# Kernel optimization log

Measured on AMD Instinct MI355X. Metric: run time of the kernel, lower is better.

## Reference

```python
import jax, jax.numpy as jnp
import numpy as np

N = 100000   # nodes
E = 1600000  # edges (avg degree 16)
D = 128      # in_dim


def setup_inputs() -> dict:
    key = jax.random.key(0)
    k = jax.random.split(key, 8)
    h = jax.random.normal(k[0], (N, D), dtype=jnp.float32)
    d = jax.random.uniform(k[1], (N,), dtype=jnp.float32)  # per-node degree norm (e.g. deg^-0.5)
    yes_no = jax.random.uniform(k[2], (E,), dtype=jnp.float32)
    gate_w = jax.random.normal(k[3], (1, 2 * D), dtype=jnp.float32) * (1.414 / np.sqrt(2 * D))
    gate_b = jnp.zeros((1,), dtype=jnp.float32)
    yes_weight = jax.random.uniform(k[4], (), dtype=jnp.float32)
    no_weight = jax.random.uniform(k[5], (), dtype=jnp.float32)
    src = jax.random.randint(k[6], (E,), 0, N, dtype=jnp.int64)
    dst = jax.random.randint(k[7], (E,), 0, N, dtype=jnp.int64)
    return {"h": h, "d": d, "yes_no": yes_no, "gate_w": gate_w, "gate_b": gate_b,
            "yes_weight": yes_weight, "no_weight": no_weight, "src": src, "dst": dst}


def reference(h, d, yes_no, gate_w, gate_b, yes_weight, no_weight, src, dst):
    n, dim = h.shape
    # gate(cat[h_dst, h_src]) == h_dst @ W[:, :D].T + h_src @ W[:, D:].T + b
    # project once per node, then gather per edge (avoids [E, 2D] concat)
    p_dst = h @ gate_w[0, :dim]  # [N]
    p_src = h @ gate_w[0, dim:]  # [N]
    g = jnp.tanh(p_dst[dst] + p_src[src] + gate_b[0])  # [E]
    yn = jnp.tanh(yes_no * yes_weight + (1.0 - yes_no) * no_weight)  # [E]
    e = (g + yn) * 0.5 * d[dst] * d[src]  # [E] (dropout p=0 -> identity)
    m = h[src] * e[:, None]  # [E, D] edge messages
    z = jax.ops.segment_sum(m, dst, num_segments=n)  # [N, D]
    return z
```

## Files before the change

kernel.cpp:

```cpp
#include <hip/hip_runtime.h>

#define D 128
#define CAP 64
#define NPB 250
#define NBMAX 512
#define EPB 4096
#define BCAP 5120

__device__ __forceinline__ unsigned short f2bf(float x) {
    unsigned int u = __float_as_uint(x);
    u += 0x7FFFu + ((u >> 16) & 1u);
    return (unsigned short)(u >> 16);
}
__device__ __forceinline__ float bf2f(unsigned short b) {
    return __uint_as_float(((unsigned int)b) << 16);
}

__global__ __launch_bounds__(256) void proj_kernel(const float* __restrict__ h,
                                                   const float* __restrict__ gw,
                                                   const float* __restrict__ dnorm,
                                                   float4* __restrict__ q,
                                                   unsigned short* __restrict__ hb,
                                                   unsigned int* __restrict__ tails,
                                                   int n_nodes) {
    if (blockIdx.x == 0) {
        tails[threadIdx.x] = 0u;
        tails[threadIdx.x + 256] = 0u;
    }
    int node = (int)((blockIdx.x * blockDim.x + threadIdx.x) >> 6);
    int lane = threadIdx.x & 63;
    if (node >= n_nodes) return;
    const float2* hr2 = (const float2*)(h + (size_t)node * D);
    const float2* gw2 = (const float2*)gw;
    float2 hv = hr2[lane];
    float2 wa = gw2[lane];
    float2 wb = gw2[lane + 64];
    ushort2 hvb = make_ushort2(f2bf(hv.x), f2bf(hv.y));
    *(ushort2*)(hb + (size_t)node * D + 2 * lane) = hvb;
    float s1 = hv.x * wa.x + hv.y * wa.y;
    float s2 = hv.x * wb.x + hv.y * wb.y;
    #pragma unroll
    for (int off = 32; off > 0; off >>= 1) {
        s1 += __shfl_down(s1, off, 64);
        s2 += __shfl_down(s2, off, 64);
    }
    if (lane == 0) q[node] = make_float4(s1, s2, dnorm[node], 0.0f);
}

__global__ __launch_bounds__(512) void bin_kernel(const float4* __restrict__ q,
                                                  const float* __restrict__ yes_no,
                                                  const int* __restrict__ src,
                                                  const int* __restrict__ dst,
                                                  const float* __restrict__ gate_b,
                                                  const float* __restrict__ yes_w,
                                                  const float* __restrict__ no_w,
                                                  unsigned int* __restrict__ tails,
                                                  unsigned long long* __restrict__ recs,
                                                  int n_edges, int nb) {
    __shared__ unsigned long long sorted[EPB];
    __shared__ unsigned int hist[NBMAX];
    __shared__ unsigned int sbuf[NBMAX];
    __shared__ unsigned int base[NBMAX];
    __shared__ unsigned int cursor[NBMAX];
    __shared__ unsigned int gbase[NBMAX];

    int tid = threadIdx.x;
    int e0 = blockIdx.x * EPB;
    int n = n_edges - e0;
    if (n > EPB) n = EPB;

    hist[tid] = 0u;
    __syncthreads();

    for (int j = tid; j < n; j += 512) {
        unsigned int d = (unsigned int)dst[e0 + j];
        atomicAdd(&hist[d / NPB], 1u);
    }
    __syncthreads();

    sbuf[tid] = hist[tid];
    __syncthreads();
    unsigned int* pa = sbuf;
    unsigned int* pb = gbase;
    #pragma unroll
    for (int s = 1; s < NBMAX; s <<= 1) {
        unsigned int v = pa[tid] + ((tid >= s) ? pa[tid - s] : 0u);
        pb[tid] = v;
        __syncthreads();
        unsigned int* t = pa; pa = pb; pb = t;
    }
    unsigned int ex = (tid == 0) ? 0u : pa[tid - 1];
    base[tid] = ex;
    cursor[tid] = ex;
    __syncthreads();

    float gb = gate_b[0];
    float yw = yes_w[0];
    float nw = no_w[0];

    for (int j = tid; j < n; j += 512) {
        int e = e0 + j;
        int dd = dst[e];
        int ss = src[e];
        float yn = yes_no[e];
        float4 qt = q[dd];
        float4 qs = q[ss];
        float g = tanhf(qt.x + qs.y + gb);
        float y = tanhf(yn * yw + (1.0f - yn) * nw);
        float ce = (g + y) * 0.5f * qt.z * qs.z;
        int qv = (int)rintf(ce * 8191.0f) + 8192;
        unsigned int w0 = ((unsigned int)ss << 15) | (unsigned int)qv;
        unsigned int bk = (unsigned int)dd / NPB;
        unsigned int pos = atomicAdd(&cursor[bk], 1u);
        sorted[pos] = ((unsigned long long)(unsigned int)dd << 32) | (unsigned long long)w0;
    }
    __syncthreads();

    gbase[tid] = (hist[tid] > 0u) ? atomicAdd(&tails[tid], hist[tid]) : 0u;
    __syncthreads();

    for (int j = tid; j < n; j += 512) {
        unsigned long long r = sorted[j];
        unsigned int bk = (unsigned int)(r >> 32) / NPB;
        unsigned int gpos = gbase[bk] + ((unsigned int)j - base[bk]);
        if (gpos < BCAP)
            __builtin_nontemporal_store(r, recs + (size_t)bk * BCAP + gpos);
    }
}

__global__ __launch_bounds__(256) void scatter_kernel(const unsigned int* __restrict__ tails,
                                                      const unsigned long long* __restrict__ recs,
                                                      int* __restrict__ cnt,
                                                      unsigned int* __restrict__ csr,
                                                      int n_nodes) {
    __shared__ unsigned int sw0[BCAP];
    __shared__ unsigned char snl[BCAP];
    __shared__ unsigned int hist2[256];
    __shared__ unsigned int sa[256];
    __shared__ unsigned int sb[256];
    __shared__ unsigned int rowbase[256];
    __shared__ unsigned int cursor2[256];

    int b = blockIdx.x;
    int tid = threadIdx.x;
    unsigned int nrec = tails[b];
    if (nrec > BCAP) nrec = BCAP;
    const unsigned long long* rb = recs + (size_t)b * BCAP;
    int node0 = b * NPB;

    hist2[tid] = 0u;
    __syncthreads();

    for (unsigned int j = tid; j < nrec; j += 256) {
        unsigned long long r = __builtin_nontemporal_load(rb + j);
        unsigned int nl = (unsigned int)(r >> 32) - (unsigned int)node0;
        atomicAdd(&hist2[nl], 1u);
    }
    __syncthreads();

    sa[tid] = hist2[tid];
    __syncthreads();
    unsigned int* pa = sa;
    unsigned int* pb = sb;
    #pragma unroll
    for (int s = 1; s < 256; s <<= 1) {
        unsigned int v = pa[tid] + ((tid >= s) ? pa[tid - s] : 0u);
        pb[tid] = v;
        __syncthreads();
        unsigned int* t = pa; pa = pb; pb = t;
    }
    unsigned int ex = (tid == 0) ? 0u : pa[tid - 1];
    rowbase[tid] = ex;
    cursor2[tid] = ex;
    __syncthreads();

    for (unsigned int j = tid; j < nrec; j += 256) {
        unsigned long long r = rb[j];
        unsigned int nl = (unsigned int)(r >> 32) - (unsigned int)node0;
        unsigned int pos = atomicAdd(&cursor2[nl], 1u);
        sw0[pos] = (unsigned int)r;
        snl[pos] = (unsigned char)nl;
    }
    __syncthreads();

    for (unsigned int j = tid; j < nrec; j += 256) {
        unsigned int nl = snl[j];
        unsigned int k = j - rowbase[nl];
        if (k < CAP)
            csr[(size_t)(node0 + (int)nl) * CAP + k] = sw0[j];
    }
    if (tid < NPB && node0 + tid < n_nodes)
        cnt[node0 + tid] = (int)hist2[tid];
}

__global__ __launch_bounds__(256) void gather_kernel(const unsigned short* __restrict__ hb,
                                                     const int* __restrict__ cnt,
                                                     const unsigned int* __restrict__ csr,
                                                     float4* __restrict__ z4,
                                                     int n_nodes) {
    int node = (int)((blockIdx.x * blockDim.x + threadIdx.x) >> 5);
    int lane = threadIdx.x & 31;
    if (node >= n_nodes) return;
    int n = cnt[node];
    if (n > CAP) n = CAP;
    const unsigned int* row = csr + (size_t)node * CAP;
    float4 acc = make_float4(0.0f, 0.0f, 0.0f, 0.0f);
    const float inv = 1.0f / 8191.0f;
    int k = 0;
    for (; k + 3 < n; k += 4) {
        unsigned int e0 = row[k], e1 = row[k + 1], e2 = row[k + 2], e3 = row[k + 3];
        float c0 = (float)((int)(e0 & 0x7fffu) - 8192) * inv;
        float c1 = (float)((int)(e1 & 0x7fffu) - 8192) * inv;
        float c2 = (float)((int)(e2 & 0x7fffu) - 8192) * inv;
        float c3 = (float)((int)(e3 & 0x7fffu) - 8192) * inv;
        ushort4 a = *(const ushort4*)(hb + (size_t)(e0 >> 15) * D + 4 * lane);
        ushort4 b = *(const ushort4*)(hb + (size_t)(e1 >> 15) * D + 4 * lane);
        ushort4 c = *(const ushort4*)(hb + (size_t)(e2 >> 15) * D + 4 * lane);
        ushort4 d = *(const ushort4*)(hb + (size_t)(e3 >> 15) * D + 4 * lane);
        acc.x += bf2f(a.x) * c0 + bf2f(b.x) * c1 + bf2f(c.x) * c2 + bf2f(d.x) * c3;
        acc.y += bf2f(a.y) * c0 + bf2f(b.y) * c1 + bf2f(c.y) * c2 + bf2f(d.y) * c3;
        acc.z += bf2f(a.z) * c0 + bf2f(b.z) * c1 + bf2f(c.z) * c2 + bf2f(d.z) * c3;
        acc.w += bf2f(a.w) * c0 + bf2f(b.w) * c1 + bf2f(c.w) * c2 + bf2f(d.w) * c3;
    }
    for (; k < n; ++k) {
        unsigned int e0 = row[k];
        float c0 = (float)((int)(e0 & 0x7fffu) - 8192) * inv;
        ushort4 a = *(const ushort4*)(hb + (size_t)(e0 >> 15) * D + 4 * lane);
        acc.x += bf2f(a.x) * c0;
        acc.y += bf2f(a.y) * c0;
        acc.z += bf2f(a.z) * c0;
        acc.w += bf2f(a.w) * c0;
    }
    z4[(size_t)node * (D / 4) + lane] = acc;
}

extern "C" void kernel_launch(void* const* d_in, const int* in_sizes, int n_in,
                              void* d_out, int out_size, void* d_ws, size_t ws_size,
                              hipStream_t stream) {
    const float* h       = (const float*)d_in[0];
    const float* dnorm   = (const float*)d_in[1];
    const float* yes_no  = (const float*)d_in[2];
    const float* gate_w  = (const float*)d_in[3];
    const float* gate_b  = (const float*)d_in[4];
    const float* yes_w   = (const float*)d_in[5];
    const float* no_w    = (const float*)d_in[6];
    const int*   src     = (const int*)d_in[7];
    const int*   dst     = (const int*)d_in[8];

    int n_nodes = in_sizes[0] / D;
    int n_edges = in_sizes[2];
    int nb = (n_nodes + NPB - 1) / NPB;

    char* ws = (char*)d_ws;
    size_t off = 0;
    auto take = [&](size_t bytes) {
        void* ptr = ws + off;
        off += (bytes + 15) & ~(size_t)15;
        return ptr;
    };
    float4*             q     = (float4*)take((size_t)n_nodes * sizeof(float4));
    unsigned short*     hb    = (unsigned short*)take((size_t)n_nodes * D * sizeof(unsigned short));
    int*                cnt   = (int*)take((size_t)n_nodes * sizeof(int));
    unsigned int*       csr   = (unsigned int*)take((size_t)n_nodes * CAP * sizeof(unsigned int));
    unsigned int*       tails = (unsigned int*)take((size_t)NBMAX * sizeof(unsigned int));
    unsigned long long* recs  = (unsigned long long*)take((size_t)nb * BCAP * sizeof(unsigned long long));
    (void)ws_size;

    proj_kernel<<<(n_nodes + 3) / 4, 256, 0, stream>>>(h, gate_w, dnorm, q, hb, tails, n_nodes);

    bin_kernel<<<(n_edges + EPB - 1) / EPB, 512, 0, stream>>>(
        q, yes_no, src, dst, gate_b, yes_w, no_w, tails, recs, n_edges, nb);

    scatter_kernel<<<nb, 256, 0, stream>>>(tails, recs, cnt, csr, n_nodes);

    gather_kernel<<<(n_nodes + 7) / 8, 256, 0, stream>>>(
        hb, cnt, csr, (float4*)d_out, n_nodes);
}
```

Measured before the change: 259.6 us.

## Widen gather loads to 16 bytes, use fast tanh, halve edges per bin block

The gather kernel now uses 16 lanes per node, with each lane loading 8 bf16 values (16 bytes) instead of 4. This halves the number of load instructions per row and doubles the number of nodes per block. Both tanh calls in the bin kernel now use an exp-plus-reciprocal approximation. Edges per bin block drop from 4096 to 2048, which doubles the number of blocks. Together these aim at memory-instruction overhead, transcendental cost and load balance, at the cost of slightly lower tanh accuracy and more atomic traffic on the bucket tails.

```diff
diff --git a/kernel.cpp b/kernel.cpp
--- a/kernel.cpp
+++ b/kernel.cpp
@@ -4,8 +4,11 @@
 #define CAP 64
 #define NPB 250
 #define NBMAX 512
-#define EPB 4096
+#define EPB 2048
 #define BCAP 5120
+
+typedef unsigned short u16x8 __attribute__((ext_vector_type(8)));
+typedef float          f32x8 __attribute__((ext_vector_type(8)));
 
 __device__ __forceinline__ unsigned short f2bf(float x) {
     unsigned int u = __float_as_uint(x);
@@ -14,6 +17,10 @@
 }
 __device__ __forceinline__ float bf2f(unsigned short b) {
     return __uint_as_float(((unsigned int)b) << 16);
+}
+__device__ __forceinline__ float fast_tanh(float x) {
+    float e = __expf(2.0f * x);
+    return 1.0f - 2.0f * __builtin_amdgcn_rcpf(e + 1.0f);
 }
 
 __global__ __launch_bounds__(256) void proj_kernel(const float* __restrict__ h,
@@ -105,8 +112,8 @@
         float yn = yes_no[e];
         float4 qt = q[dd];
         float4 qs = q[ss];
-        float g = tanhf(qt.x + qs.y + gb);
-        float y = tanhf(yn * yw + (1.0f - yn) * nw);
+        float g = fast_tanh(qt.x + qs.y + gb);
+        float y = fast_tanh(yn * yw + (1.0f - yn) * nw);
         float ce = (g + y) * 0.5f * qt.z * qs.z;
         int qv = (int)rintf(ce * 8191.0f) + 8192;
         unsigned int w0 = ((unsigned int)ss << 15) | (unsigned int)qv;
@@ -198,13 +205,14 @@
                                                      const unsigned int* __restrict__ csr,
                                                      float4* __restrict__ z4,
                                                      int n_nodes) {
-    int node = (int)((blockIdx.x * blockDim.x + threadIdx.x) >> 5);
-    int lane = threadIdx.x & 31;
+    int node = (int)((blockIdx.x * blockDim.x + threadIdx.x) >> 4);
+    int lane = threadIdx.x & 15;
     if (node >= n_nodes) return;
     int n = cnt[node];
     if (n > CAP) n = CAP;
     const unsigned int* row = csr + (size_t)node * CAP;
-    float4 acc = make_float4(0.0f, 0.0f, 0.0f, 0.0f);
+    const unsigned short* hbl = hb + 8 * lane;
+    f32x8 acc = (f32x8)0.0f;
     const float inv = 1.0f / 8191.0f;
     int k = 0;
     for (; k + 3 < n; k += 4) {
@@ -213,25 +221,26 @@
         float c1 = (float)((int)(e1 & 0x7fffu) - 8192) * inv;
         float c2 = (float)((int)(e2 & 0x7fffu) - 8192) * inv;
         float c3 = (float)((int)(e3 & 0x7fffu) - 8192) * inv;
-        ushort4 a = *(const ushort4*)(hb + (size_t)(e0 >> 15) * D + 4 * lane);
-        ushort4 b = *(const ushort4*)(hb + (size_t)(e1 >> 15) * D + 4 * lane);
-        ushort4 c = *(const ushort4*)(hb + (size_t)(e2 >> 15) * D + 4 * lane);
-        ushort4 d = *(const ushort4*)(hb + (size_t)(e3 >> 15) * D + 4 * lane);
-        acc.x += bf2f(a.x) * c0 + bf2f(b.x) * c1 + bf2f(c.x) * c2 + bf2f(d.x) * c3;
-        acc.y += bf2f(a.y) * c0 + bf2f(b.y) * c1 + bf2f(c.y) * c2 + bf2f(d.y) * c3;
-        acc.z += bf2f(a.z) * c0 + bf2f(b.z) * c1 + bf2f(c.z) * c2 + bf2f(d.z) * c3;
-        acc.w += bf2f(a.w) * c0 + bf2f(b.w) * c1 + bf2f(c.w) * c2 + bf2f(d.w) * c3;
+        u16x8 a = *(const u16x8*)(hbl + (size_t)(e0 >> 15) * D);
+        u16x8 b = *(const u16x8*)(hbl + (size_t)(e1 >> 15) * D);
+        u16x8 c = *(const u16x8*)(hbl + (size_t)(e2 >> 15) * D);
+        u16x8 d = *(const u16x8*)(hbl + (size_t)(e3 >> 15) * D);
+        #pragma unroll
+        for (int j = 0; j < 8; ++j) {
+            acc[j] += bf2f(a[j]) * c0 + bf2f(b[j]) * c1 + bf2f(c[j]) * c2 + bf2f(d[j]) * c3;
+        }
     }
     for (; k < n; ++k) {
         unsigned int e0 = row[k];
         float c0 = (float)((int)(e0 & 0x7fffu) - 8192) * inv;
-        ushort4 a = *(const ushort4*)(hb + (size_t)(e0 >> 15) * D + 4 * lane);
-        acc.x += bf2f(a.x) * c0;
-        acc.y += bf2f(a.y) * c0;
-        acc.z += bf2f(a.z) * c0;
-        acc.w += bf2f(a.w) * c0;
-    }
-    z4[(size_t)node * (D / 4) + lane] = acc;
+        u16x8 a = *(const u16x8*)(hbl + (size_t)(e0 >> 15) * D);
+        #pragma unroll
+        for (int j = 0; j < 8; ++j) acc[j] += bf2f(a[j]) * c0;
+    }
+    float4 lo = make_float4(acc[0], acc[1], acc[2], acc[3]);
+    float4 hi = make_float4(acc[4], acc[5], acc[6], acc[7]);
+    z4[(size_t)node * (D / 4) + 2 * lane]     = lo;
+    z4[(size_t)node * (D / 4) + 2 * lane + 1] = hi;
 }
 
 extern "C" void kernel_launch(void* const* d_in, const int* in_sizes, int n_in,
@@ -273,6 +282,6 @@
 
     scatter_kernel<<<nb, 256, 0, stream>>>(tails, recs, cnt, csr, n_nodes);
 
-    gather_kernel<<<(n_nodes + 7) / 8, 256, 0, stream>>>(
+    gather_kernel<<<(n_nodes + 15) / 16, 256, 0, stream>>>(
         hb, cnt, csr, (float4*)d_out, n_nodes);
 }
```

New measurement: 255.1 us. About the same (-1.7%).
